# Optimization experiments

Hardware: AMD Instinct MI355X
Metric: run time of the kernel (lower is better)

Reference implementation:

```python
import jax, jax.numpy as jnp
import numpy as np

HIDDEN = 4096
N_HEADS = 32
N_KV_HEADS = 8
HEAD_DIM = HIDDEN // N_HEADS  # 128
ROPE_THETA = 10000.0


def rotate_half(x):
    x1, x2 = jnp.split(x, 2, axis=-1)
    return jnp.concatenate((-x2, x1), axis=-1)


def rope_cos_sin(seq_len, dim, theta, dtype):
    inv_freq = 1.0 / (theta ** (jnp.arange(0, dim, 2, dtype=jnp.float32) / dim))
    t = jnp.arange(seq_len, dtype=jnp.float32)
    freqs = jnp.outer(t, inv_freq)               # [S, D/2]
    emb = jnp.concatenate((freqs, freqs), axis=-1)  # [S, D]
    return jnp.cos(emb).astype(dtype), jnp.sin(emb).astype(dtype)


def setup_inputs() -> dict:
    key = jax.random.key(0)
    k0, k1, k2, k3, k4 = jax.random.split(key, 5)
    B, S = 1, 2048
    std = 1.0 / np.sqrt(HIDDEN)
    return {
        "hidden_states": jax.random.normal(k0, (B, S, HIDDEN), dtype=jnp.float32),
        "wq": jax.random.normal(k1, (N_HEADS * HEAD_DIM, HIDDEN), dtype=jnp.float32) * std,
        "wk": jax.random.normal(k2, (N_KV_HEADS * HEAD_DIM, HIDDEN), dtype=jnp.float32) * std,
        "wv": jax.random.normal(k3, (N_KV_HEADS * HEAD_DIM, HIDDEN), dtype=jnp.float32) * std,
        "wo": jax.random.normal(k4, (HIDDEN, N_HEADS * HEAD_DIM), dtype=jnp.float32) * std,
    }


def reference(hidden_states, wq, wk, wv, wo):
    B, S, _ = hidden_states.shape
    dtype = hidden_states.dtype
    G = N_HEADS // N_KV_HEADS  # query groups per kv head

    # projections (torch Linear: x @ W.T)
    q = (hidden_states @ wq.T).reshape(B, S, N_HEADS, HEAD_DIM).transpose(0, 2, 1, 3)      # [B,H,S,D]
    k = (hidden_states @ wk.T).reshape(B, S, N_KV_HEADS, HEAD_DIM).transpose(0, 2, 1, 3)   # [B,Hkv,S,D]
    v = (hidden_states @ wv.T).reshape(B, S, N_KV_HEADS, HEAD_DIM).transpose(0, 2, 1, 3)   # [B,Hkv,S,D]

    cos, sin = rope_cos_sin(S, HEAD_DIM, ROPE_THETA, dtype)  # [S,D]
    cos = cos[None, None]  # [1,1,S,D]
    sin = sin[None, None]
    q = q * cos + rotate_half(q) * sin
    k = k * cos + rotate_half(k) * sin

    # GQA: group query heads with their kv head (equivalent to repeat_interleave on kv)
    qg = q.reshape(B, N_KV_HEADS, G, S, HEAD_DIM)
    scale = 1.0 / np.sqrt(HEAD_DIM)
    scores = jnp.einsum("bkgsd,bktd->bkgst", qg, k) * scale  # [B,Hkv,G,S,S]

    causal = jnp.tril(jnp.ones((S, S), dtype=bool))
    scores = jnp.where(causal, scores, -jnp.inf)
    probs = jax.nn.softmax(scores.astype(jnp.float32), axis=-1).astype(dtype)

    out = jnp.einsum("bkgst,bktd->bkgsd", probs, v)  # [B,Hkv,G,S,D]
    out = out.reshape(B, N_HEADS, S, HEAD_DIM).transpose(0, 2, 1, 3).reshape(B, S, N_HEADS * HEAD_DIM)
    return out @ wo.T
```

## Files before the change

kernel.cpp:

```cpp
#include <hip/hip_runtime.h>
#include <hip/hip_bf16.h>


typedef _Float16 half4_t __attribute__((ext_vector_type(4)));
typedef _Float16 half8_t __attribute__((ext_vector_type(8)));
typedef float f32x4 __attribute__((ext_vector_type(4)));

#define S_LEN 2048
#define HID 4096
#define NH 32
#define NKV 8

__device__ __forceinline__ void gload_lds16(const void* g, void* l) {
  __builtin_amdgcn_global_load_lds((const __attribute__((address_space(1))) void*)g,
                                   (__attribute__((address_space(3))) void*)l, 16, 0, 0);
}

__global__ __launch_bounds__(256) void cvt_f32_f16(const float* __restrict__ src,
                                                   _Float16* __restrict__ dst, int n4) {
  int i = blockIdx.x * 256 + threadIdx.x;
  if (i >= n4) return;
  f32x4 v = *(const f32x4*)(src + (size_t)i * 4);
  half4_t h = {(_Float16)v[0], (_Float16)v[1], (_Float16)v[2], (_Float16)v[3]};
  *(half4_t*)(dst + (size_t)i * 4) = h;
}

__global__ __launch_bounds__(256) void cvt_qkv(const float* __restrict__ wq,
                                               const float* __restrict__ wk,
                                               const float* __restrict__ wv,
                                               _Float16* __restrict__ dst, int n4) {
  int i = blockIdx.x * 256 + threadIdx.x;
  if (i >= n4) return;
  size_t e = (size_t)i * 4;
  const float* src;
  size_t off;
  if (e < (size_t)4096 * 4096)      { src = wq; off = e; }
  else if (e < (size_t)5120 * 4096) { src = wk; off = e - (size_t)4096 * 4096; }
  else                              { src = wv; off = e - (size_t)5120 * 4096; }
  f32x4 v = *(const f32x4*)(src + off);
  half4_t h = {(_Float16)v[0], (_Float16)v[1], (_Float16)v[2], (_Float16)v[3]};
  *(half4_t*)(dst + e) = h;
}

__global__ __launch_bounds__(256) void rope_table_kernel(float* __restrict__ cost,
                                                         float* __restrict__ sint) {
  int i = blockIdx.x * 256 + threadIdx.x;
  int d = i & 63;
  int s = i >> 6;
  float inv = exp2f(-(float)d * (13.287712379549449f / 64.0f));
  float f = (float)s * inv;
  cost[i] = cosf(f);
  sint[i] = sinf(f);
}

__global__ __launch_bounds__(256) void rope_apply_q(_Float16* __restrict__ X,
                                                    const float* __restrict__ cost,
                                                    const float* __restrict__ sint) {
  int idx = blockIdx.x * 256 + threadIdx.x;
  int g = idx & 15;
  int tmp = idx >> 4;
  int h = tmp % NH;
  int s = tmp / NH;
  int d0 = g * 4;
  size_t base = (size_t)s * HID + h * 128 + d0;
  half4_t x1 = *(half4_t*)(X + base);
  half4_t x2 = *(half4_t*)(X + base + 64);
  const float* cp = cost + s * 64 + d0;
  const float* sp = sint + s * 64 + d0;
  half4_t y1, y2;
#pragma unroll
  for (int j = 0; j < 4; ++j) {
    float c = cp[j], sn = sp[j];
    float a = (float)x1[j], b = (float)x2[j];
    y1[j] = (_Float16)(a * c - b * sn);
    y2[j] = (_Float16)(b * c + a * sn);
  }
  *(half4_t*)(X + base) = y1;
  *(half4_t*)(X + base + 64) = y2;
}

__global__ __launch_bounds__(256) void rope_k2_inplace(_Float16* __restrict__ K2,
                                                       const float* __restrict__ cost,
                                                       const float* __restrict__ sint) {
  int idx = blockIdx.x * 256 + threadIdx.x;
  int g = idx & 15;
  int tmp = idx >> 4;
  int h = tmp % NKV;
  int s = tmp / NKV;
  int d0 = g * 4;
  size_t tb = (size_t)h * (S_LEN * 128) + (size_t)(s >> 4) * 2048 + (size_t)(s & 15) * 8;
  size_t a1 = tb + (size_t)(d0 >> 3) * 128 + (d0 & 7);
  size_t a2 = a1 + 1024;
  half4_t x1 = *(half4_t*)(K2 + a1);
  half4_t x2 = *(half4_t*)(K2 + a2);
  const float* cp = cost + s * 64 + d0;
  const float* sp = sint + s * 64 + d0;
  half4_t y1, y2;
#pragma unroll
  for (int j = 0; j < 4; ++j) {
    float c = cp[j], sn = sp[j];
    float a = (float)x1[j], b = (float)x2[j];
    y1[j] = (_Float16)(a * c - b * sn);
    y2[j] = (_Float16)(b * c + a * sn);
  }
  *(half4_t*)(K2 + a1) = y1;
  *(half4_t*)(K2 + a2) = y2;
}

template <int MODE>
__global__ __launch_bounds__(512, 2) void gemm8(const _Float16* __restrict__ A,
                                                const _Float16* __restrict__ W,
                                                void* __restrict__ out,
                                                _Float16* __restrict__ K2,
                                                _Float16* __restrict__ V2) {
  __shared__ __align__(16) _Float16 As[2][2][128 * 64];
  __shared__ __align__(16) _Float16 Bs[2][2][128 * 64];
  const int t = threadIdx.x;
  const int wid = t >> 6, l = t & 63, lr = l & 15, lg = l >> 4;
  const int wm = wid >> 2, wn = wid & 3;
  const int m0 = blockIdx.y * 256, n0 = blockIdx.x * 256;
  const int NT = 4096 / 64;

  const _Float16* Abase = A + (size_t)m0 * 4096;
  const _Float16* Wbase = W + (size_t)n0 * 4096;

  f32x4 acc[8][4] = {};
  half8_t af[4][2], bf[4][2];

#define STAGE_A(buf_, kb_)                                                              \
  _Pragma("unroll") for (int hh = 0; hh < 2; ++hh)                                      \
  _Pragma("unroll") for (int j = 0; j < 2; ++j) {                                       \
    const int ciw = j * 512 + wid * 64;                           \
    const int ci = ciw + l;                                                             \
    const int r = ci >> 3, c8 = ci & 7;                                                 \
    gload_lds16(Abase + (size_t)(hh * 128 + r) * 4096 + (kb_) + ((c8 ^ (r & 7)) << 3),  \
                &As[buf_][hh][ciw * 8]);                                                \
  }
#define STAGE_B(buf_, kb_)                                                              \
  _Pragma("unroll") for (int hh = 0; hh < 2; ++hh)                                      \
  _Pragma("unroll") for (int j = 0; j < 2; ++j) {                                       \
    const int ciw = j * 512 + wid * 64;                                                 \
    const int ci = ciw + l;                                                             \
    const int r = ci >> 3, c8 = ci & 7;                                                 \
    gload_lds16(Wbase + (size_t)(hh * 128 + r) * 4096 + (kb_) + ((c8 ^ (r & 7)) << 3),  \
                &Bs[buf_][hh][ciw * 8]);                                                \
  }
#define LDA(mlo_)                                                                       \
  _Pragma("unroll") for (int mi = 0; mi < 4; ++mi)                                      \
  _Pragma("unroll") for (int kk = 0; kk < 2; ++kk) {                                    \
    const int c8 = (kk * 4 + lg) ^ (lr & 7);                                            \
    af[mi][kk] = *(const half8_t*)&As[cur][wm][(((mlo_) + mi) * 16 + lr) * 64 + c8 * 8];\
  }
#define LDB(nlo_)                                                                       \
  _Pragma("unroll") for (int ni = 0; ni < 2; ++ni)                                      \
  _Pragma("unroll") for (int kk = 0; kk < 2; ++kk) {                                    \
    const int c8 = (kk * 4 + lg) ^ (lr & 7);                                            \
    bf[(nlo_) + ni][kk] = *(const half8_t*)&Bs[cur][wn >> 1]                            \
        [((wn & 1) * 64 + ((nlo_) + ni) * 16 + lr) * 64 + c8 * 8];                      \
  }
#define MFMA16(mlo_, nlo_)                                                              \
  _Pragma("unroll") for (int mi = 0; mi < 4; ++mi)                                      \
  _Pragma("unroll") for (int ni = 0; ni < 2; ++ni)                                      \
  _Pragma("unroll") for (int kk = 0; kk < 2; ++kk)                                      \
    acc[(mlo_) + mi][(nlo_) + ni] = __builtin_amdgcn_mfma_f32_16x16x32_f16(             \
        af[mi][kk], bf[(nlo_) + ni][kk], acc[(mlo_) + mi][(nlo_) + ni], 0, 0, 0);

  STAGE_A(0, 0)
  STAGE_B(0, 0)
  asm volatile("s_waitcnt vmcnt(0)" ::: "memory");
  __builtin_amdgcn_sched_barrier(0);
  __builtin_amdgcn_s_barrier();

  int cur = 0;
  for (int kt = 0; kt < NT; ++kt) {
    const int nkb = (kt + 1) << 6;
    const bool pre = (kt + 1 < NT);
    LDA(0)
    LDB(0)
    if (pre) { STAGE_A(cur ^ 1, nkb) }
    __builtin_amdgcn_sched_barrier(0);
    __builtin_amdgcn_s_barrier();
    __builtin_amdgcn_s_setprio(1);
    MFMA16(0, 0)
    __builtin_amdgcn_s_setprio(0);
    __builtin_amdgcn_sched_barrier(0);
    __builtin_amdgcn_s_barrier();
    LDB(2)
    if (pre) { STAGE_B(cur ^ 1, nkb) }
    __builtin_amdgcn_sched_barrier(0);
    __builtin_amdgcn_s_barrier();
    __builtin_amdgcn_s_setprio(1);
    MFMA16(0, 2)
    __builtin_amdgcn_s_setprio(0);
    __builtin_amdgcn_sched_barrier(0);
    __builtin_amdgcn_s_barrier();
    LDA(4)
    __builtin_amdgcn_sched_barrier(0);
    __builtin_amdgcn_s_barrier();
    __builtin_amdgcn_s_setprio(1);
    MFMA16(4, 2)
    __builtin_amdgcn_s_setprio(0);
    __builtin_amdgcn_sched_barrier(0);
    __builtin_amdgcn_s_barrier();
    __builtin_amdgcn_s_setprio(1);
    MFMA16(4, 0)
    __builtin_amdgcn_s_setprio(0);
    asm volatile("s_waitcnt vmcnt(0)" ::: "memory");
    __builtin_amdgcn_sched_barrier(0);
    __builtin_amdgcn_s_barrier();
    cur ^= 1;
  }
#undef STAGE_A
#undef STAGE_B
#undef LDA
#undef LDB
#undef MFMA16

  const int grow0 = m0 + wm * 128;
  const int gcol0 = n0 + wn * 64;
#pragma unroll
  for (int mi = 0; mi < 8; ++mi) {
#pragma unroll
    for (int ni = 0; ni < 4; ++ni) {
      const int row = grow0 + mi * 16 + lg * 4;
      const int col = gcol0 + ni * 16 + lr;
      if (MODE == 1) {
#pragma unroll
        for (int i = 0; i < 4; ++i)
          ((float*)out)[(size_t)(row + i) * 4096 + col] = acc[mi][ni][i];
      } else {
        if (col < 4096) {
#pragma unroll
          for (int i = 0; i < 4; ++i)
            ((_Float16*)out)[(size_t)(row + i) * 4096 + col] = (_Float16)acc[mi][ni][i];
        } else if (col < 5120) {
          const int c = col - 4096;
          const int h = c >> 7, d = c & 127;
          const size_t kb2 = (size_t)h * (S_LEN * 128) + (size_t)(row >> 4) * 2048 +
                             (size_t)(d >> 3) * 128 + (d & 7);
#pragma unroll
          for (int i = 0; i < 4; ++i)
            K2[kb2 + ((row + i) & 15) * 8] = (_Float16)acc[mi][ni][i];
        } else {
          const int c = col - 5120;
          half4_t o;
#pragma unroll
          for (int i = 0; i < 4; ++i) o[i] = (_Float16)acc[mi][ni][i];
          *(half4_t*)(V2 + (size_t)(c >> 7) * (S_LEN * 128) + (size_t)(row >> 4) * 2048 +
                      (size_t)(c & 127) * 16 + (row & 15)) = o;
        }
      }
    }
  }
}

__global__ __launch_bounds__(256) void attn_kernel(const _Float16* __restrict__ Q,
                                                   const _Float16* __restrict__ K2,
                                                   const _Float16* __restrict__ V2,
                                                   _Float16* __restrict__ Op,
                                                   float* __restrict__ Md) {
  const int bid = blockIdx.x;
  const int hk = bid & 7;
  const int split = (bid >> 3) & 1;
  const int qt = 63 - (bid >> 4);
  const int w = threadIdx.x >> 6;
  const int h = hk * 4 + w;
  const int l = threadIdx.x & 63;
  const int lr = l & 15;
  const int lg = l >> 4;
  const float scale = 0.08838834764831845f;
  const float LOG2E = 1.4426950408889634f;
  const float NEG = -1.0e30f;

  const int half_steps = qt + 1;
  const int kt0 = split * half_steps;
  const int kt1 = kt0 + half_steps;

  int sq[2];
  half8_t qf[2][4];
#pragma unroll
  for (int qc = 0; qc < 2; ++qc) {
    sq[qc] = qt * 32 + qc * 16 + lr;
#pragma unroll
    for (int c = 0; c < 4; ++c)
      qf[qc][c] = *(const half8_t*)(Q + (size_t)sq[qc] * HID + h * 128 + c * 32 + lg * 8);
  }
  const _Float16* Kb = K2 + (size_t)hk * (S_LEN * 128);
  const _Float16* Vb = V2 + (size_t)hk * (S_LEN * 128);

  f32x4 acc[8][2] = {};
  float m[2] = {NEG, NEG};
  float den[2] = {0.f, 0.f};

  for (int kt = kt0; kt < kt1; ++kt) {
    half8_t kf[4];
#pragma unroll
    for (int c = 0; c < 4; ++c)
      kf[c] = *(const half8_t*)(Kb + (size_t)kt * 2048 + (c * 4 + lg) * 128 + lr * 8);
    f32x4 s0 = {0.f, 0.f, 0.f, 0.f}, s1 = {0.f, 0.f, 0.f, 0.f};
#pragma unroll
    for (int c = 0; c < 4; ++c) {
      s0 = __builtin_amdgcn_mfma_f32_16x16x32_f16(kf[c], qf[0][c], s0, 0, 0, 0);
      s1 = __builtin_amdgcn_mfma_f32_16x16x32_f16(kf[c], qf[1][c], s1, 0, 0, 0);
    }
    const int kbase = kt * 16 + lg * 4;
    float sc[2][4];
#pragma unroll
    for (int i = 0; i < 4; ++i) {
      sc[0][i] = s0[i] * scale;
      sc[1][i] = s1[i] * scale;
    }
    if (kt >= 2 * qt) {
#pragma unroll
      for (int qc = 0; qc < 2; ++qc)
#pragma unroll
        for (int i = 0; i < 4; ++i)
          if (kbase + i > sq[qc]) sc[qc][i] = NEG;
    }
    half4_t pf[2];
#pragma unroll
    for (int qc = 0; qc < 2; ++qc) {
      float mx = fmaxf(fmaxf(sc[qc][0], sc[qc][1]), fmaxf(sc[qc][2], sc[qc][3]));
      mx = fmaxf(mx, __shfl_xor(mx, 16));
      mx = fmaxf(mx, __shfl_xor(mx, 32));
      if (!__all(mx - m[qc] <= 8.0f)) {
        float mn = fmaxf(m[qc], mx);
        float corr = exp2f((m[qc] - mn) * LOG2E);
        den[qc] *= corr;
#pragma unroll
        for (int dc = 0; dc < 8; ++dc)
#pragma unroll
          for (int i = 0; i < 4; ++i) acc[dc][qc][i] *= corr;
        m[qc] = mn;
      }
      float ps = 0.f, p[4];
#pragma unroll
      for (int i = 0; i < 4; ++i) {
        p[i] = exp2f((sc[qc][i] - m[qc]) * LOG2E);
        ps += p[i];
      }
      ps += __shfl_xor(ps, 16);
      ps += __shfl_xor(ps, 32);
      den[qc] += ps;
      pf[qc] = (half4_t){(_Float16)p[0], (_Float16)p[1], (_Float16)p[2], (_Float16)p[3]};
    }
#pragma unroll
    for (int dc = 0; dc < 8; ++dc) {
      half4_t vf = *(const half4_t*)(Vb + (size_t)kt * 2048 + (dc * 16 + lr) * 16 + lg * 4);
      acc[dc][0] = __builtin_amdgcn_mfma_f32_16x16x16f16(vf, pf[0], acc[dc][0], 0, 0, 0);
      acc[dc][1] = __builtin_amdgcn_mfma_f32_16x16x16f16(vf, pf[1], acc[dc][1], 0, 0, 0);
    }
  }

  _Float16* Os = Op + (size_t)split * S_LEN * HID;
#pragma unroll
  for (int qc = 0; qc < 2; ++qc) {
    float inv = den[qc] > 0.f ? 1.0f / den[qc] : 0.f;
#pragma unroll
    for (int dc = 0; dc < 8; ++dc) {
      half4_t o;
#pragma unroll
      for (int i = 0; i < 4; ++i) o[i] = (_Float16)(acc[dc][qc][i] * inv);
      *(half4_t*)(Os + (size_t)sq[qc] * HID + h * 128 + dc * 16 + lg * 4) = o;
    }
    if (lg == 0) {
      int mdix = ((split * S_LEN + sq[qc]) * NH + h) * 2;
      Md[mdix] = m[qc];
      Md[mdix + 1] = den[qc];
    }
  }
}

__global__ __launch_bounds__(256) void attn_combine(const _Float16* __restrict__ Op,
                                                    const float* __restrict__ Md,
                                                    _Float16* __restrict__ O) {
  const float LOG2E = 1.4426950408889634f;
  int idx = blockIdx.x * 256 + threadIdx.x;
  int dd = (idx & 15) * 8;
  int h = (idx >> 4) & 31;
  int s = idx >> 9;
  int base = (s * NH + h) * 2;
  float m0 = Md[base], den0 = Md[base + 1];
  float m1 = Md[S_LEN * NH * 2 + base], den1 = Md[S_LEN * NH * 2 + base + 1];
  float M = fmaxf(m0, m1);
  float w0 = den0 * exp2f((m0 - M) * LOG2E);
  float w1 = den1 * exp2f((m1 - M) * LOG2E);
  float r = 1.0f / (w0 + w1);
  w0 *= r;
  w1 *= r;
  size_t off = (size_t)s * HID + h * 128 + dd;
  half8_t a = *(const half8_t*)(Op + off);
  half8_t b = *(const half8_t*)(Op + (size_t)S_LEN * HID + off);
  half8_t o;
#pragma unroll
  for (int j = 0; j < 8; ++j) o[j] = (_Float16)(w0 * (float)a[j] + w1 * (float)b[j]);
  *(half8_t*)(O + off) = o;
}

extern "C" void kernel_launch(void* const* d_in, const int* in_sizes, int n_in,
                              void* d_out, int out_size, void* d_ws, size_t ws_size,
                              hipStream_t stream) {
  (void)in_sizes; (void)n_in; (void)out_size; (void)ws_size;
  const float* hs = (const float*)d_in[0];
  const float* wq = (const float*)d_in[1];
  const float* wk = (const float*)d_in[2];
  const float* wv = (const float*)d_in[3];
  const float* wo = (const float*)d_in[4];

  char* ws = (char*)d_ws;
  _Float16* hs_h = (_Float16*)(ws);
  _Float16* q_h  = (_Float16*)(ws + (16u << 20));
  _Float16* K2   = (_Float16*)(ws + (32u << 20));
  _Float16* V2   = (_Float16*)(ws + (36u << 20));
  float* cost    = (float*)(ws + (40u << 20));
  float* sint    = (float*)(ws + (40u << 20) + (512u << 10));
  _Float16* wqkv = (_Float16*)(ws + (41u << 20));
  _Float16* Op   = wqkv;
  float* Md      = (float*)(ws + (73u << 20));
  _Float16* wo_h = wqkv;
  _Float16* o_h  = hs_h;

  cvt_f32_f16<<<8192, 256, 0, stream>>>(hs, hs_h, (S_LEN * HID) / 4);
  rope_table_kernel<<<(S_LEN * 64) / 256, 256, 0, stream>>>(cost, sint);
  cvt_qkv<<<24576, 256, 0, stream>>>(wq, wk, wv, wqkv, (6144 * 4096) / 4);

  gemm8<0><<<dim3(24, 8), 512, 0, stream>>>(hs_h, wqkv, q_h, K2, V2);

  rope_apply_q<<<(S_LEN * NH * 16) / 256, 256, 0, stream>>>(q_h, cost, sint);
  rope_k2_inplace<<<(S_LEN * NKV * 16) / 256, 256, 0, stream>>>(K2, cost, sint);

  attn_kernel<<<1024, 256, 0, stream>>>(q_h, K2, V2, Op, Md);
  attn_combine<<<4096, 256, 0, stream>>>(Op, Md, o_h);

  cvt_f32_f16<<<16384, 256, 0, stream>>>(wo, wo_h, (HID * HID) / 4);
  gemm8<1><<<dim3(16, 8), 512, 0, stream>>>(o_h, wo_h, d_out, nullptr, nullptr);
}
```

Measured before the change: 399.4 us.

## Restructure GEMM main loop into finer-grained half-tile load/compute pipeline

Rewrites the GEMM k-loop so that global-to-LDS staging is split into half-tile chunks, interleaved with four MFMA quadrants and unrolled by two iterations. A/B buffer refills are issued earlier, with partial vmcnt waits in place of full drains, and the A fragment register array doubles to hold both halves. Launch bounds drop to one block per CU, allowing more registers at the cost of occupancy. The aim is better overlap of memory latency with MFMA work, in exchange for more barriers and a more delicate hazard ordering.

```diff
diff --git a/kernel.cpp b/kernel.cpp
--- a/kernel.cpp
+++ b/kernel.cpp
@@ -108,7 +108,7 @@
 }
 
 template <int MODE>
-__global__ __launch_bounds__(512, 2) void gemm8(const _Float16* __restrict__ A,
+__global__ __launch_bounds__(512, 1) void gemmP(const _Float16* __restrict__ A,
                                                 const _Float16* __restrict__ W,
                                                 void* __restrict__ out,
                                                 _Float16* __restrict__ K2,
@@ -119,102 +119,145 @@
   const int wid = t >> 6, l = t & 63, lr = l & 15, lg = l >> 4;
   const int wm = wid >> 2, wn = wid & 3;
   const int m0 = blockIdx.y * 256, n0 = blockIdx.x * 256;
-  const int NT = 4096 / 64;
 
   const _Float16* Abase = A + (size_t)m0 * 4096;
   const _Float16* Wbase = W + (size_t)n0 * 4096;
 
   f32x4 acc[8][4] = {};
-  half8_t af[4][2], bf[4][2];
-
-#define STAGE_A(buf_, kb_)                                                              \
-  _Pragma("unroll") for (int hh = 0; hh < 2; ++hh)                                      \
-  _Pragma("unroll") for (int j = 0; j < 2; ++j) {                                       \
-    const int ciw = j * 512 + wid * 64;                           \
-    const int ci = ciw + l;                                                             \
-    const int r = ci >> 3, c8 = ci & 7;                                                 \
-    gload_lds16(Abase + (size_t)(hh * 128 + r) * 4096 + (kb_) + ((c8 ^ (r & 7)) << 3),  \
-                &As[buf_][hh][ciw * 8]);                                                \
-  }
-#define STAGE_B(buf_, kb_)                                                              \
-  _Pragma("unroll") for (int hh = 0; hh < 2; ++hh)                                      \
-  _Pragma("unroll") for (int j = 0; j < 2; ++j) {                                       \
-    const int ciw = j * 512 + wid * 64;                                                 \
-    const int ci = ciw + l;                                                             \
-    const int r = ci >> 3, c8 = ci & 7;                                                 \
-    gload_lds16(Wbase + (size_t)(hh * 128 + r) * 4096 + (kb_) + ((c8 ^ (r & 7)) << 3),  \
-                &Bs[buf_][hh][ciw * 8]);                                                \
-  }
-#define LDA(mlo_)                                                                       \
-  _Pragma("unroll") for (int mi = 0; mi < 4; ++mi)                                      \
-  _Pragma("unroll") for (int kk = 0; kk < 2; ++kk) {                                    \
-    const int c8 = (kk * 4 + lg) ^ (lr & 7);                                            \
-    af[mi][kk] = *(const half8_t*)&As[cur][wm][(((mlo_) + mi) * 16 + lr) * 64 + c8 * 8];\
-  }
-#define LDB(nlo_)                                                                       \
-  _Pragma("unroll") for (int ni = 0; ni < 2; ++ni)                                      \
-  _Pragma("unroll") for (int kk = 0; kk < 2; ++kk) {                                    \
-    const int c8 = (kk * 4 + lg) ^ (lr & 7);                                            \
-    bf[(nlo_) + ni][kk] = *(const half8_t*)&Bs[cur][wn >> 1]                            \
-        [((wn & 1) * 64 + ((nlo_) + ni) * 16 + lr) * 64 + c8 * 8];                      \
-  }
-#define MFMA16(mlo_, nlo_)                                                              \
-  _Pragma("unroll") for (int mi = 0; mi < 4; ++mi)                                      \
-  _Pragma("unroll") for (int ni = 0; ni < 2; ++ni)                                      \
-  _Pragma("unroll") for (int kk = 0; kk < 2; ++kk)                                      \
-    acc[(mlo_) + mi][(nlo_) + ni] = __builtin_amdgcn_mfma_f32_16x16x32_f16(             \
-        af[mi][kk], bf[(nlo_) + ni][kk], acc[(mlo_) + mi][(nlo_) + ni], 0, 0, 0);
-
-  STAGE_A(0, 0)
-  STAGE_B(0, 0)
-  asm volatile("s_waitcnt vmcnt(0)" ::: "memory");
-  __builtin_amdgcn_sched_barrier(0);
-  __builtin_amdgcn_s_barrier();
-
-  int cur = 0;
-  for (int kt = 0; kt < NT; ++kt) {
-    const int nkb = (kt + 1) << 6;
-    const bool pre = (kt + 1 < NT);
-    LDA(0)
-    LDB(0)
-    if (pre) { STAGE_A(cur ^ 1, nkb) }
-    __builtin_amdgcn_sched_barrier(0);
-    __builtin_amdgcn_s_barrier();
-    __builtin_amdgcn_s_setprio(1);
-    MFMA16(0, 0)
-    __builtin_amdgcn_s_setprio(0);
-    __builtin_amdgcn_sched_barrier(0);
-    __builtin_amdgcn_s_barrier();
-    LDB(2)
-    if (pre) { STAGE_B(cur ^ 1, nkb) }
-    __builtin_amdgcn_sched_barrier(0);
-    __builtin_amdgcn_s_barrier();
-    __builtin_amdgcn_s_setprio(1);
-    MFMA16(0, 2)
-    __builtin_amdgcn_s_setprio(0);
-    __builtin_amdgcn_sched_barrier(0);
-    __builtin_amdgcn_s_barrier();
-    LDA(4)
-    __builtin_amdgcn_sched_barrier(0);
-    __builtin_amdgcn_s_barrier();
-    __builtin_amdgcn_s_setprio(1);
-    MFMA16(4, 2)
-    __builtin_amdgcn_s_setprio(0);
-    __builtin_amdgcn_sched_barrier(0);
-    __builtin_amdgcn_s_barrier();
-    __builtin_amdgcn_s_setprio(1);
-    MFMA16(4, 0)
-    __builtin_amdgcn_s_setprio(0);
+  half8_t af[8][2], bf[4][2];
+
+  const int ciw0 = wid * 64;
+  const int ciw1 = 512 + wid * 64;
+
+#define STAGE_AH(buf_, hh_, kb_)                                                         \
+  {                                                                                      \
+    { const int ci = ciw0 + l, r = ci >> 3, c8 = ci & 7;                                 \
+      gload_lds16(Abase + (size_t)((hh_)*128 + r) * 4096 + (kb_) + ((c8 ^ (r & 7)) << 3),\
+                  &As[buf_][hh_][ciw0 * 8]); }                                           \
+    { const int ci = ciw1 + l, r = ci >> 3, c8 = ci & 7;                                 \
+      gload_lds16(Abase + (size_t)((hh_)*128 + r) * 4096 + (kb_) + ((c8 ^ (r & 7)) << 3),\
+                  &As[buf_][hh_][ciw1 * 8]); }                                           \
+  }
+#define STAGE_BH(buf_, hh_, kb_)                                                         \
+  {                                                                                      \
+    { const int ci = ciw0 + l, r = ci >> 3, c8 = ci & 7;                                 \
+      gload_lds16(Wbase + (size_t)((hh_)*128 + r) * 4096 + (kb_) + ((c8 ^ (r & 7)) << 3),\
+                  &Bs[buf_][hh_][ciw0 * 8]); }                                           \
+    { const int ci = ciw1 + l, r = ci >> 3, c8 = ci & 7;                                 \
+      gload_lds16(Wbase + (size_t)((hh_)*128 + r) * 4096 + (kb_) + ((c8 ^ (r & 7)) << 3),\
+                  &Bs[buf_][hh_][ciw1 * 8]); }                                           \
+  }
+#define LDA_L(buf_)                                                                      \
+  _Pragma("unroll") for (int mi = 0; mi < 4; ++mi)                                       \
+  _Pragma("unroll") for (int kk = 0; kk < 2; ++kk) {                                     \
+    const int c8 = (kk * 4 + lg) ^ (lr & 7);                                             \
+    af[mi][kk] = *(const half8_t*)&As[buf_][wm][(mi * 16 + lr) * 64 + c8 * 8];           \
+  }
+#define LDA_H(buf_)                                                                      \
+  _Pragma("unroll") for (int mi = 0; mi < 4; ++mi)                                       \
+  _Pragma("unroll") for (int kk = 0; kk < 2; ++kk) {                                     \
+    const int c8 = (kk * 4 + lg) ^ (lr & 7);                                             \
+    af[4 + mi][kk] = *(const half8_t*)&As[buf_][wm][((4 + mi) * 16 + lr) * 64 + c8 * 8]; \
+  }
+#define LDB_L(buf_)                                                                      \
+  _Pragma("unroll") for (int ni = 0; ni < 2; ++ni)                                       \
+  _Pragma("unroll") for (int kk = 0; kk < 2; ++kk) {                                     \
+    const int c8 = (kk * 4 + lg) ^ (lr & 7);                                             \
+    bf[ni][kk] = *(const half8_t*)&Bs[buf_][wn >> 1]                                     \
+        [((wn & 1) * 64 + ni * 16 + lr) * 64 + c8 * 8];                                  \
+  }
+#define LDB_H(buf_)                                                                      \
+  _Pragma("unroll") for (int ni = 0; ni < 2; ++ni)                                       \
+  _Pragma("unroll") for (int kk = 0; kk < 2; ++kk) {                                     \
+    const int c8 = (kk * 4 + lg) ^ (lr & 7);                                             \
+    bf[2 + ni][kk] = *(const half8_t*)&Bs[buf_][wn >> 1]                                 \
+        [((wn & 1) * 64 + (2 + ni) * 16 + lr) * 64 + c8 * 8];                            \
+  }
+#define QUAD(mlo_, nlo_)                                                                 \
+  _Pragma("unroll") for (int mi = 0; mi < 4; ++mi)                                       \
+  _Pragma("unroll") for (int ni = 0; ni < 2; ++ni)                                       \
+  _Pragma("unroll") for (int kk = 0; kk < 2; ++kk)                                       \
+    acc[(mlo_) + mi][(nlo_) + ni] = __builtin_amdgcn_mfma_f32_16x16x32_f16(              \
+        af[(mlo_) + mi][kk], bf[(nlo_) + ni][kk], acc[(mlo_) + mi][(nlo_) + ni], 0, 0, 0);
+#define SB __builtin_amdgcn_sched_barrier(0)
+#define BARR __builtin_amdgcn_s_barrier()
+#define LGKM0 asm volatile("s_waitcnt lgkmcnt(0)" ::: "memory")
+#define PRI1 __builtin_amdgcn_s_setprio(1)
+#define PRI0 __builtin_amdgcn_s_setprio(0)
+
+  STAGE_AH(0, 0, 0) STAGE_AH(0, 1, 0) STAGE_BH(0, 0, 0) STAGE_BH(0, 1, 0)
+  STAGE_AH(1, 0, 64) STAGE_AH(1, 1, 64)
+  asm volatile("s_waitcnt vmcnt(4)" ::: "memory");
+  SB; BARR;
+
+  for (int i = 0; i < 31; ++i) {
+    const int kb1 = (2 * i + 1) * 64, kb2 = (2 * i + 2) * 64, kb3 = (2 * i + 3) * 64;
+    LDA_L(0) LDB_L(0) STAGE_BH(1, 0, kb1)
+    SB; BARR; LGKM0; SB;
+    PRI1; QUAD(0, 0) PRI0; SB; BARR;
+    LDA_H(0) STAGE_BH(1, 1, kb1)
+    SB; BARR; LGKM0; SB;
+    PRI1; QUAD(4, 0) PRI0; SB; BARR;
+    LDB_H(0) STAGE_AH(0, 0, kb2)
+    SB; BARR; LGKM0; SB;
+    PRI1; QUAD(0, 2) PRI0; SB; BARR;
+    STAGE_AH(0, 1, kb2)
+    SB; BARR;
+    PRI1; QUAD(4, 2) PRI0;
+    asm volatile("s_waitcnt vmcnt(4)" ::: "memory");
+    SB; BARR;
+    LDA_L(1) LDB_L(1) STAGE_BH(0, 0, kb2)
+    SB; BARR; LGKM0; SB;
+    PRI1; QUAD(0, 0) PRI0; SB; BARR;
+    LDA_H(1) STAGE_BH(0, 1, kb2)
+    SB; BARR; LGKM0; SB;
+    PRI1; QUAD(4, 0) PRI0; SB; BARR;
+    LDB_H(1) STAGE_AH(1, 0, kb3)
+    SB; BARR; LGKM0; SB;
+    PRI1; QUAD(0, 2) PRI0; SB; BARR;
+    STAGE_AH(1, 1, kb3)
+    SB; BARR;
+    PRI1; QUAD(4, 2) PRI0;
+    asm volatile("s_waitcnt vmcnt(4)" ::: "memory");
+    SB; BARR;
+  }
+  {
+    const int kb1 = 63 * 64;
+    LDA_L(0) LDB_L(0) STAGE_BH(1, 0, kb1)
+    SB; BARR; LGKM0; SB;
+    PRI1; QUAD(0, 0) PRI0; SB; BARR;
+    LDA_H(0) STAGE_BH(1, 1, kb1)
+    SB; BARR; LGKM0; SB;
+    PRI1; QUAD(4, 0) PRI0; SB; BARR;
+    LDB_H(0)
+    SB; BARR; LGKM0; SB;
+    PRI1; QUAD(0, 2) PRI0; SB; BARR;
+    PRI1; QUAD(4, 2) PRI0;
     asm volatile("s_waitcnt vmcnt(0)" ::: "memory");
-    __builtin_amdgcn_sched_barrier(0);
-    __builtin_amdgcn_s_barrier();
-    cur ^= 1;
-  }
-#undef STAGE_A
-#undef STAGE_B
-#undef LDA
-#undef LDB
-#undef MFMA16
+    SB; BARR;
+    LDA_L(1) LDB_L(1)
+    SB; BARR; LGKM0; SB;
+    PRI1; QUAD(0, 0) PRI0; SB; BARR;
+    LDA_H(1)
+    SB; BARR; LGKM0; SB;
+    PRI1; QUAD(4, 0) PRI0; SB; BARR;
+    LDB_H(1)
+    SB; BARR; LGKM0; SB;
+    PRI1; QUAD(0, 2) PRI0; SB; BARR;
+    PRI1; QUAD(4, 2) PRI0;
+  }
+#undef STAGE_AH
+#undef STAGE_BH
+#undef LDA_L
+#undef LDA_H
+#undef LDB_L
+#undef LDB_H
+#undef QUAD
+#undef SB
+#undef BARR
+#undef LGKM0
+#undef PRI1
+#undef PRI0
 
   const int grow0 = m0 + wm * 128;
   const int gcol0 = n0 + wn * 64;
@@ -424,7 +467,7 @@
   rope_table_kernel<<<(S_LEN * 64) / 256, 256, 0, stream>>>(cost, sint);
   cvt_qkv<<<24576, 256, 0, stream>>>(wq, wk, wv, wqkv, (6144 * 4096) / 4);
 
-  gemm8<0><<<dim3(24, 8), 512, 0, stream>>>(hs_h, wqkv, q_h, K2, V2);
+  gemmP<0><<<dim3(24, 8), 512, 0, stream>>>(hs_h, wqkv, q_h, K2, V2);
 
   rope_apply_q<<<(S_LEN * NH * 16) / 256, 256, 0, stream>>>(q_h, cost, sint);
   rope_k2_inplace<<<(S_LEN * NKV * 16) / 256, 256, 0, stream>>>(K2, cost, sint);
@@ -433,5 +476,5 @@
   attn_combine<<<4096, 256, 0, stream>>>(Op, Md, o_h);
 
   cvt_f32_f16<<<16384, 256, 0, stream>>>(wo, wo_h, (HID * HID) / 4);
-  gemm8<1><<<dim3(16, 8), 512, 0, stream>>>(o_h, wo_h, d_out, nullptr, nullptr);
-}
+  gemmP<1><<<dim3(16, 8), 512, 0, stream>>>(o_h, wo_h, d_out, nullptr, nullptr);
+}
```

Result: slower. 415.6 us (+4.0%).
